# Kernel optimization log

Hardware: AMD Instinct MI355X
Metric: run time of the kernel (lower is better)

Reference implementation:

```python
import jax, jax.numpy as jnp
import numpy as np

B, L, d, D = 256, 128, 2, 128  # batch, sites, local dim, bond dim


def setup_inputs() -> dict:
    key = jax.random.key(0)
    k1, k2 = jax.random.split(key)
    # local quantum-number indices (output of hilbert.states_to_local_indices)
    x = jax.random.randint(k1, (B, L), 0, d, dtype=jnp.int32)
    # MPS unit-cell tensors: kernel_init (normal, std=0.01) + identity, as in setup()
    tensors = 0.01 * jax.random.normal(k2, (L, d, D, D), dtype=jnp.float32) \
        + jnp.eye(D, dtype=jnp.float32)
    return {"x": x, "tensors": tensors}


def reference(x, tensors):
    # x: (B, L) int indices in [0, d); tensors: (L, d, D, D)
    # symperiod == L so the tile in __call__ is a no-op.
    Bn, Ln = x.shape
    Dn = tensors.shape[-1]
    edge0 = jnp.broadcast_to(jnp.eye(Dn, dtype=tensors.dtype), (Bn, Dn, Dn))

    @jax.checkpoint
    def step(edge, pair):
        site_tensors, qn = pair          # (d, D, D), (B,)
        a = site_tensors[qn]             # gather per-sample matrix -> (B, D, D)
        return edge @ a, None            # batched (B,D,D)@(B,D,D)

    edge, _ = jax.lax.scan(step, edge0, (tensors, x.T))
    psi = jnp.trace(edge, axis1=-2, axis2=-1)     # (B,)
    return jnp.log(psi.astype(jnp.complex64))
```

## Files before the change

### kernel.cpp

```cpp
#include <hip/hip_runtime.h>
#include <cstdint>

#define DD   128
#define LL   128
#define MAT  (DD*DD)
#define ROWB 256

typedef float  f32x16 __attribute__((ext_vector_type(16)));
typedef short  bf16x8 __attribute__((ext_vector_type(8)));
typedef unsigned short u16_t;

__device__ u16_t g_A  [LL*2*MAT];
__device__ u16_t g_At [LL*2*MAT];
__device__ u16_t g_M2 [64*4*MAT];
__device__ u16_t g_M2t[64*4*MAT];
__device__ u16_t g_M4t[32*16*MAT];
__device__ u16_t g_F0 [256*MAT];
__device__ u16_t g_F1 [256*MAT];

__device__ __forceinline__ u16_t f2bf(float f){
  unsigned int x = __builtin_bit_cast(unsigned int, f);
  unsigned int r = (x + 0x7FFFu + ((x >> 16) & 1u)) >> 16;
  return (u16_t)r;
}
__device__ __forceinline__ float bf2f(u16_t u){
  unsigned int x = ((unsigned int)u) << 16;
  return __builtin_bit_cast(float, x);
}
__device__ __forceinline__ f32x16 mfma32(bf16x8 a, bf16x8 b, f32x16 c){
  return __builtin_amdgcn_mfma_f32_32x32x16_bf16(a, b, c, 0, 0, 0);
}
__device__ __forceinline__ f32x16 zero16(){
  f32x16 z;
#pragma unroll
  for (int i = 0; i < 16; ++i) z[i] = 0.f;
  return z;
}
__device__ __forceinline__ unsigned cvtpk(float lo, float hi){
  unsigned r;
  asm("v_cvt_pk_bf16_f32 %0, %1, %2" : "=v"(r) : "v"(lo), "v"(hi));
  return r;
}
__device__ __forceinline__ void pl32swap(unsigned &a, unsigned &b){
  asm volatile("v_permlane32_swap_b32 %0, %1" : "+v"(a), "+v"(b));
}

__device__ __forceinline__ void stage32k(char* dstLds, const u16_t* srcG, int ltid){
  int w4 = ltid >> 6, l = ltid & 63;
  const char* g = (const char*)srcG + w4*8192 + l*16;
  char* s = dstLds + w4*8192;
#pragma unroll
  for (int i = 0; i < 8; ++i){
    __builtin_amdgcn_global_load_lds(
      (const __attribute__((address_space(1))) unsigned int*)(uintptr_t)(g + i*1024),
      (__attribute__((address_space(3))) unsigned int*)(unsigned int)(uintptr_t)(s + i*1024),
      16, 0, 0);
  }
}

__global__ __launch_bounds__(256, 1) void k_convert(const float* __restrict__ T){
  __shared__ float tile[128][129];
  const int lq = blockIdx.x, tid = threadIdx.x;
  const float* src = T + (size_t)lq * MAT;
#pragma unroll 4
  for (int i = 0; i < 64; ++i){
    int idx = tid + 256*i;
    float v = src[idx];
    g_A[lq*MAT + idx] = f2bf(v);
    tile[idx >> 7][idx & 127] = v;
  }
  __syncthreads();
#pragma unroll 4
  for (int i = 0; i < 64; ++i){
    int idx = tid + 256*i;
    int c = idx >> 7, k = idx & 127;
    g_At[lq*MAT + idx] = f2bf(tile[k][c]);
  }
}

__global__ __launch_bounds__(256, 1) void k_prod(int level){
  __shared__ u16_t CT[MAT];
  __shared__ u16_t CR[MAT];
  const int bid = blockIdx.x, tid = threadIdx.x;
  const int w = tid >> 6, lane = tid & 63, g = lane >> 5, ln = lane & 31;
  const int wr = (w >> 1) * 64, wc = (w & 1) * 64;

  const u16_t *X, *Yt; u16_t *Z, *Zt;
  if (level == 1){
    int p = bid >> 2, c2 = bid & 3;
    X  = g_A  + ((2*p)*2   + (c2 & 1)) * MAT;
    Yt = g_At + ((2*p+1)*2 + ((c2 >> 1) & 1)) * MAT;
    Z  = g_M2  + bid*MAT;
    Zt = g_M2t + bid*MAT;
  } else {
    int gg = bid >> 4, c = bid & 15;
    X  = g_M2  + ((2*gg)*4   + (c & 3)) * MAT;
    Yt = g_M2t + ((2*gg+1)*4 + (c >> 2)) * MAT;
    Z  = nullptr;
    Zt = g_M4t + bid*MAT;
  }

  f32x16 acc[2][2];
  acc[0][0] = zero16(); acc[0][1] = zero16();
  acc[1][0] = zero16(); acc[1][1] = zero16();

#pragma unroll
  for (int kw = 0; kw < 8; ++kw){
    int ko = kw*32 + g*16;
    bf16x8 a0 = *(const bf16x8*)((const char*)X  + (wr + ln     )*ROWB + ko);
    bf16x8 a1 = *(const bf16x8*)((const char*)X  + (wr + 32 + ln)*ROWB + ko);
    bf16x8 b0 = *(const bf16x8*)((const char*)Yt + (wc + ln     )*ROWB + ko);
    bf16x8 b1 = *(const bf16x8*)((const char*)Yt + (wc + 32 + ln)*ROWB + ko);
    acc[0][0] = mfma32(a0, b0, acc[0][0]);
    acc[0][1] = mfma32(a0, b1, acc[0][1]);
    acc[1][0] = mfma32(a1, b0, acc[1][0]);
    acc[1][1] = mfma32(a1, b1, acc[1][1]);
  }

#pragma unroll
  for (int mt = 0; mt < 2; ++mt){
#pragma unroll
    for (int nt = 0; nt < 2; ++nt){
      int c  = wc + nt*32 + ln;
      int xc = (c & 15) << 4;
#pragma unroll
      for (int q = 0; q < 4; ++q){
        int r4 = wr + mt*32 + 8*q + 4*g;
        unsigned int lo = (unsigned)f2bf(acc[mt][nt][4*q+0]) | ((unsigned)f2bf(acc[mt][nt][4*q+1]) << 16);
        unsigned int hi = (unsigned)f2bf(acc[mt][nt][4*q+2]) | ((unsigned)f2bf(acc[mt][nt][4*q+3]) << 16);
        uint2 v; v.x = lo; v.y = hi;
        *(uint2*)((char*)CT + c*ROWB + ((2*r4) ^ xc)) = v;
      }
      if (level == 1){
#pragma unroll
        for (int i = 0; i < 16; ++i){
          int r = wr + mt*32 + (i & 3) + 8*(i >> 2) + 4*g;
          *(u16_t*)((char*)CR + r*ROWB + ((2*c) ^ ((r & 15) << 4))) = f2bf(acc[mt][nt][i]);
        }
      }
    }
  }
  __syncthreads();

  if (level == 1){
#pragma unroll
    for (int i = 0; i < 8; ++i){
      int o = (tid + 256*i) * 16;
      int row = o >> 8, wb = o & 255;
      int xr = (row & 15) << 4;
      uint4 vt = *(const uint4*)((const char*)CT + row*ROWB + (wb ^ xr));
      *(uint4*)((char*)Zt + o) = vt;
      uint4 vz = *(const uint4*)((const char*)CR + row*ROWB + (wb ^ xr));
      *(uint4*)((char*)Z + o) = vz;
    }
  } else {
#pragma unroll
    for (int i = 0; i < 8; ++i){
      int o = tid + 256*i;
      int lnn = o & 31, ggg = (o >> 5) & 1, kww = (o >> 6) & 7, rtt = o >> 9;
      int r = 32*rtt + lnn;
      int srcB = r*ROWB + ((32*kww + 16*ggg) ^ ((r & 15) << 4));
      uint4 vt = *(const uint4*)((const char*)CT + srcB);
      *(uint4*)((char*)Zt + o*16) = vt;
    }
  }
}

#define LDS_MAIN (2*32768 + 64)

__global__ __launch_bounds__(256, 1) void k_main(const int* __restrict__ x){
  extern __shared__ char lds[];
  char* bufs  = lds;
  int*  combo = (int*)(lds + 2*32768);

  const int bid = blockIdx.x;
  const int b = bid & 255, half = bid >> 8;
  const int tid = threadIdx.x;
  const int w = tid >> 6, lane = tid & 63, g = lane >> 5, ln = lane & 31;

  if (tid < 16){
    const int* xb = x + b*LL + (half*16 + tid)*4;
    combo[tid] = (xb[0] & 1) | ((xb[1] & 1) << 1) | ((xb[2] & 1) << 2) | ((xb[3] & 1) << 3);
  }

  uint4 F[8];
#pragma unroll
  for (int kw = 0; kw < 8; ++kw){
    unsigned wd[4] = {0u,0u,0u,0u};
#pragma unroll
    for (int j = 0; j < 8; ++j){
      int k = 16*kw + 8*g + j;
      if (k == 32*w + ln) wd[j >> 1] |= 0x3F80u << (16*(j & 1));
    }
    uint4 v; v.x = wd[0]; v.y = wd[1]; v.z = wd[2]; v.w = wd[3];
    F[kw] = v;
  }
  __syncthreads();

  stage32k(bufs, g_M4t + (size_t)((half*16)*16 + combo[0])*MAT, tid);
  __syncthreads();

  for (int s = 0; s < 16; ++s){
    const char* Mc = bufs + (s & 1)*32768;
    char*       Mn = bufs + ((s + 1) & 1)*32768;
    if (s + 1 < 16){
      stage32k(Mn, g_M4t + (size_t)((half*16 + s + 1)*16 + combo[s+1])*MAT, tid);
    }

    const char* Ml = Mc + lane*16;

    f32x16 acc[4];
#pragma unroll
    for (int rt = 0; rt < 4; ++rt) acc[rt] = zero16();

#pragma unroll
    for (int kw = 0; kw < 8; ++kw){
      bf16x8 bb = __builtin_bit_cast(bf16x8, F[kw]);
#pragma unroll
      for (int rt = 0; rt < 4; ++rt){
        bf16x8 a = *(const bf16x8*)(Ml + (rt*8 + kw)*1024);
        acc[rt] = mfma32(a, bb, acc[rt]);
      }
    }

#pragma unroll
    for (int rt = 0; rt < 4; ++rt){
      unsigned y0 = cvtpk(acc[rt][0],  acc[rt][1]);
      unsigned x0 = cvtpk(acc[rt][4],  acc[rt][5]);
      pl32swap(y0, x0);
      unsigned y1 = cvtpk(acc[rt][2],  acc[rt][3]);
      unsigned x1 = cvtpk(acc[rt][6],  acc[rt][7]);
      pl32swap(y1, x1);
      uint4 v0; v0.x = y0; v0.y = y1; v0.z = x0; v0.w = x1;
      F[2*rt] = v0;

      unsigned y2 = cvtpk(acc[rt][8],  acc[rt][9]);
      unsigned x2 = cvtpk(acc[rt][12], acc[rt][13]);
      pl32swap(y2, x2);
      unsigned y3 = cvtpk(acc[rt][10], acc[rt][11]);
      unsigned x3 = cvtpk(acc[rt][14], acc[rt][15]);
      pl32swap(y3, x3);
      uint4 v1; v1.x = y2; v1.y = y3; v1.z = x2; v1.w = x3;
      F[2*rt+1] = v1;
    }
    __syncthreads();
  }

  const int c = 32*w + ln;
  if (half == 0){
    u16_t* dst = g_F0 + (size_t)b*MAT + c*128;
#pragma unroll
    for (int kw = 0; kw < 8; ++kw)
      *(uint4*)(dst + kw*16 + g*8) = F[kw];
  } else {
    u16_t* dst = g_F1 + (size_t)b*MAT + c;
#pragma unroll
    for (int kw = 0; kw < 8; ++kw){
      uint4 v = F[kw];
      unsigned wd[4] = {v.x, v.y, v.z, v.w};
#pragma unroll
      for (int j = 0; j < 8; ++j){
        int k = 16*kw + 8*g + j;
        u16_t bits = (u16_t)((j & 1) ? (wd[j >> 1] >> 16) : (wd[j >> 1] & 0xFFFF));
        dst[(size_t)k*128] = bits;
      }
    }
  }
}

__global__ __launch_bounds__(256, 1) void k_tail(float* __restrict__ out,
                                                 int out_complex){
  __shared__ float red[4];
  const int b = blockIdx.x, tid = threadIdx.x;
  const int w = tid >> 6, lane = tid & 63;

  const u16_t* S0 = g_F0 + (size_t)b*MAT;
  const u16_t* W  = g_F1 + (size_t)b*MAT;

  float sum = 0.f;
#pragma unroll
  for (int i = 0; i < 8; ++i){
    int o = (i*256 + tid)*8;
    uint4 a = *(const uint4*)(S0 + o);
    uint4 v = *(const uint4*)(W  + o);
    unsigned aw[4] = {a.x, a.y, a.z, a.w};
    unsigned vw[4] = {v.x, v.y, v.z, v.w};
#pragma unroll
    for (int q = 0; q < 4; ++q){
      sum += bf2f((u16_t)(aw[q] & 0xFFFF)) * bf2f((u16_t)(vw[q] & 0xFFFF));
      sum += bf2f((u16_t)(aw[q] >> 16))    * bf2f((u16_t)(vw[q] >> 16));
    }
  }
#pragma unroll
  for (int off = 1; off < 64; off <<= 1) sum += __shfl_xor(sum, off, 64);
  if (lane == 0) red[w] = sum;
  __syncthreads();
  if (tid == 0){
    float s = red[0] + red[1] + red[2] + red[3];
    float re = logf(fabsf(s));
    float im = (s < 0.f) ? 3.14159265358979323f : 0.f;
    if (out_complex){ out[2*b] = re; out[2*b+1] = im; }
    else            { out[b] = re; }
  }
}

extern "C" void kernel_launch(void* const* d_in, const int* in_sizes, int n_in,
                              void* d_out, int out_size, void* d_ws, size_t ws_size,
                              hipStream_t stream){
  const int*   x = (const int*)d_in[0];
  const float* T = (const float*)d_in[1];
  int Bn = in_sizes[0] / LL;
  int oc = (out_size >= 2*Bn) ? 1 : 0;

  (void)d_ws; (void)ws_size; (void)n_in;
  hipFuncSetAttribute(reinterpret_cast<const void*>(k_main),
                      hipFuncAttributeMaxDynamicSharedMemorySize, LDS_MAIN);

  k_convert<<<LL*2,  256, 0, stream>>>(T);
  k_prod   <<<256,   256, 0, stream>>>(1);
  k_prod   <<<512,   256, 0, stream>>>(2);
  k_main   <<<2*Bn,  256, LDS_MAIN, stream>>>(x);
  k_tail   <<<Bn,    256, 0, stream>>>((float*)d_out, oc);
}
```

Measured before the change: 76.93 us.

## Split chain product into four quarters per sample and combine with MFMA tail

Each sample's 128-site chain product is now split across four blocks of 32 sites instead of two blocks of 64. Each block streams half-matrix 16KB chunks in a double-buffered loop, with smaller LDS and launch bounds allowing four blocks per CU. The tail kernel now does two 128x128 bf16 matrix products per sample with MFMA and computes the trace of their product via elementwise dot. This raises parallelism and occupancy in the main kernel. In exchange it adds a heavier tail kernel, more global scratch traffic, and an extra bf16 rounding stage.

```diff
diff --git a/kernel.cpp b/kernel.cpp
--- a/kernel.cpp
+++ b/kernel.cpp
@@ -17,6 +17,8 @@
 __device__ u16_t g_M4t[32*16*MAT];
 __device__ u16_t g_F0 [256*MAT];
 __device__ u16_t g_F1 [256*MAT];
+__device__ u16_t g_F2 [256*MAT];
+__device__ u16_t g_F3 [256*MAT];
 
 __device__ __forceinline__ u16_t f2bf(float f){
   unsigned int x = __builtin_bit_cast(unsigned int, f);
@@ -45,12 +47,12 @@
   asm volatile("v_permlane32_swap_b32 %0, %1" : "+v"(a), "+v"(b));
 }
 
-__device__ __forceinline__ void stage32k(char* dstLds, const u16_t* srcG, int ltid){
-  int w4 = ltid >> 6, l = ltid & 63;
-  const char* g = (const char*)srcG + w4*8192 + l*16;
-  char* s = dstLds + w4*8192;
-#pragma unroll
-  for (int i = 0; i < 8; ++i){
+__device__ __forceinline__ void stage16k(char* dstLds, const u16_t* srcG, int tid){
+  int w4 = tid >> 6, l = tid & 63;
+  const char* g = (const char*)srcG + w4*4096 + l*16;
+  char* s = dstLds + w4*4096;
+#pragma unroll
+  for (int i = 0; i < 4; ++i){
     __builtin_amdgcn_global_load_lds(
       (const __attribute__((address_space(1))) unsigned int*)(uintptr_t)(g + i*1024),
       (__attribute__((address_space(3))) unsigned int*)(unsigned int)(uintptr_t)(s + i*1024),
@@ -166,22 +168,18 @@
   }
 }
 
-#define LDS_MAIN (2*32768 + 64)
-
-__global__ __launch_bounds__(256, 1) void k_main(const int* __restrict__ x){
+#define LDS_MAIN (2*16384)
+
+__global__ __launch_bounds__(256, 4) void k_main(const int* __restrict__ x){
   extern __shared__ char lds[];
-  char* bufs  = lds;
-  int*  combo = (int*)(lds + 2*32768);
 
   const int bid = blockIdx.x;
-  const int b = bid & 255, half = bid >> 8;
+  const int b = bid & 255, q = bid >> 8;
   const int tid = threadIdx.x;
   const int w = tid >> 6, lane = tid & 63, g = lane >> 5, ln = lane & 31;
 
-  if (tid < 16){
-    const int* xb = x + b*LL + (half*16 + tid)*4;
-    combo[tid] = (xb[0] & 1) | ((xb[1] & 1) << 1) | ((xb[2] & 1) << 2) | ((xb[3] & 1) << 3);
-  }
+  int xv = x[b*LL + q*32 + (lane & 31)] & 1;
+  unsigned long long bits = __ballot(xv != 0);
 
   uint4 F[8];
 #pragma unroll
@@ -195,65 +193,72 @@
     uint4 v; v.x = wd[0]; v.y = wd[1]; v.z = wd[2]; v.w = wd[3];
     F[kw] = v;
   }
+
+  {
+    int cb0 = (int)(bits & 15ull);
+    stage16k(lds, g_M4t + (size_t)((q*8)*16 + cb0)*MAT, tid);
+  }
   __syncthreads();
 
-  stage32k(bufs, g_M4t + (size_t)((half*16)*16 + combo[0])*MAT, tid);
-  __syncthreads();
-
-  for (int s = 0; s < 16; ++s){
-    const char* Mc = bufs + (s & 1)*32768;
-    char*       Mn = bufs + ((s + 1) & 1)*32768;
-    if (s + 1 < 16){
-      stage32k(Mn, g_M4t + (size_t)((half*16 + s + 1)*16 + combo[s+1])*MAT, tid);
-    }
-
-    const char* Ml = Mc + lane*16;
-
-    f32x16 acc[4];
-#pragma unroll
-    for (int rt = 0; rt < 4; ++rt) acc[rt] = zero16();
+  f32x16 acc[4];
+  for (int p = 0; p < 16; ++p){
+    if ((p & 1) == 0){
+#pragma unroll
+      for (int rt = 0; rt < 4; ++rt) acc[rt] = zero16();
+    }
+    if (p + 1 < 16){
+      int it = (p + 1) >> 1, h = (p + 1) & 1;
+      int cb = (int)((bits >> (4*it)) & 15ull);
+      stage16k(lds + ((p + 1) & 1)*16384,
+               g_M4t + (size_t)((q*8 + it)*16 + cb)*MAT + h*8192, tid);
+    }
+
+    const char* Ml = lds + (p & 1)*16384 + lane*16;
+    const int h = p & 1;
 
 #pragma unroll
     for (int kw = 0; kw < 8; ++kw){
       bf16x8 bb = __builtin_bit_cast(bf16x8, F[kw]);
 #pragma unroll
+      for (int d = 0; d < 2; ++d){
+        bf16x8 a = *(const bf16x8*)(Ml + (d*8 + kw)*1024);
+        acc[2*h + d] = mfma32(a, bb, acc[2*h + d]);
+      }
+    }
+
+    if (p & 1){
+#pragma unroll
       for (int rt = 0; rt < 4; ++rt){
-        bf16x8 a = *(const bf16x8*)(Ml + (rt*8 + kw)*1024);
-        acc[rt] = mfma32(a, bb, acc[rt]);
-      }
-    }
-
-#pragma unroll
-    for (int rt = 0; rt < 4; ++rt){
-      unsigned y0 = cvtpk(acc[rt][0],  acc[rt][1]);
-      unsigned x0 = cvtpk(acc[rt][4],  acc[rt][5]);
-      pl32swap(y0, x0);
-      unsigned y1 = cvtpk(acc[rt][2],  acc[rt][3]);
-      unsigned x1 = cvtpk(acc[rt][6],  acc[rt][7]);
-      pl32swap(y1, x1);
-      uint4 v0; v0.x = y0; v0.y = y1; v0.z = x0; v0.w = x1;
-      F[2*rt] = v0;
-
-      unsigned y2 = cvtpk(acc[rt][8],  acc[rt][9]);
-      unsigned x2 = cvtpk(acc[rt][12], acc[rt][13]);
-      pl32swap(y2, x2);
-      unsigned y3 = cvtpk(acc[rt][10], acc[rt][11]);
-      unsigned x3 = cvtpk(acc[rt][14], acc[rt][15]);
-      pl32swap(y3, x3);
-      uint4 v1; v1.x = y2; v1.y = y3; v1.z = x2; v1.w = x3;
-      F[2*rt+1] = v1;
+        unsigned y0 = cvtpk(acc[rt][0],  acc[rt][1]);
+        unsigned x0 = cvtpk(acc[rt][4],  acc[rt][5]);
+        pl32swap(y0, x0);
+        unsigned y1 = cvtpk(acc[rt][2],  acc[rt][3]);
+        unsigned x1 = cvtpk(acc[rt][6],  acc[rt][7]);
+        pl32swap(y1, x1);
+        uint4 v0; v0.x = y0; v0.y = y1; v0.z = x0; v0.w = x1;
+        F[2*rt] = v0;
+
+        unsigned y2 = cvtpk(acc[rt][8],  acc[rt][9]);
+        unsigned x2 = cvtpk(acc[rt][12], acc[rt][13]);
+        pl32swap(y2, x2);
+        unsigned y3 = cvtpk(acc[rt][10], acc[rt][11]);
+        unsigned x3 = cvtpk(acc[rt][14], acc[rt][15]);
+        pl32swap(y3, x3);
+        uint4 v1; v1.x = y2; v1.y = y3; v1.z = x2; v1.w = x3;
+        F[2*rt+1] = v1;
+      }
     }
     __syncthreads();
   }
 
   const int c = 32*w + ln;
-  if (half == 0){
-    u16_t* dst = g_F0 + (size_t)b*MAT + c*128;
+  if ((q & 1) == 0){
+    u16_t* dst = (q == 0 ? g_F0 : g_F2) + (size_t)b*MAT + c*128;
 #pragma unroll
     for (int kw = 0; kw < 8; ++kw)
       *(uint4*)(dst + kw*16 + g*8) = F[kw];
   } else {
-    u16_t* dst = g_F1 + (size_t)b*MAT + c;
+    u16_t* dst = (q == 1 ? g_F1 : g_F3) + (size_t)b*MAT + c;
 #pragma unroll
     for (int kw = 0; kw < 8; ++kw){
       uint4 v = F[kw];
@@ -261,36 +266,62 @@
 #pragma unroll
       for (int j = 0; j < 8; ++j){
         int k = 16*kw + 8*g + j;
-        u16_t bits = (u16_t)((j & 1) ? (wd[j >> 1] >> 16) : (wd[j >> 1] & 0xFFFF));
-        dst[(size_t)k*128] = bits;
-      }
-    }
-  }
-}
-
-__global__ __launch_bounds__(256, 1) void k_tail(float* __restrict__ out,
-                                                 int out_complex){
+        u16_t bb = (u16_t)((j & 1) ? (wd[j >> 1] >> 16) : (wd[j >> 1] & 0xFFFF));
+        dst[(size_t)k*128] = bb;
+      }
+    }
+  }
+}
+
+__global__ __launch_bounds__(256, 1) void k_tail2(float* __restrict__ out,
+                                                  int out_complex){
   __shared__ float red[4];
   const int b = blockIdx.x, tid = threadIdx.x;
-  const int w = tid >> 6, lane = tid & 63;
-
-  const u16_t* S0 = g_F0 + (size_t)b*MAT;
-  const u16_t* W  = g_F1 + (size_t)b*MAT;
+  const int w = tid >> 6, lane = tid & 63, g = lane >> 5, ln = lane & 31;
+  const int wr = (w >> 1) * 64, wc = (w & 1) * 64;
+
+  const u16_t* X1  = g_F0 + (size_t)b*MAT;
+  const u16_t* Y1t = g_F1 + (size_t)b*MAT;
+  const u16_t* X2  = g_F3 + (size_t)b*MAT;
+  const u16_t* Y2t = g_F2 + (size_t)b*MAT;
+
+  f32x16 ap[2][2], ar[2][2];
+#pragma unroll
+  for (int mt = 0; mt < 2; ++mt)
+#pragma unroll
+    for (int nt = 0; nt < 2; ++nt){ ap[mt][nt] = zero16(); ar[mt][nt] = zero16(); }
+
+#pragma unroll
+  for (int kw = 0; kw < 8; ++kw){
+    int ko = kw*32 + g*16;
+    bf16x8 a0 = *(const bf16x8*)((const char*)X1  + (wr + ln     )*ROWB + ko);
+    bf16x8 a1 = *(const bf16x8*)((const char*)X1  + (wr + 32 + ln)*ROWB + ko);
+    bf16x8 b0 = *(const bf16x8*)((const char*)Y1t + (wc + ln     )*ROWB + ko);
+    bf16x8 b1 = *(const bf16x8*)((const char*)Y1t + (wc + 32 + ln)*ROWB + ko);
+    ap[0][0] = mfma32(a0, b0, ap[0][0]);
+    ap[0][1] = mfma32(a0, b1, ap[0][1]);
+    ap[1][0] = mfma32(a1, b0, ap[1][0]);
+    ap[1][1] = mfma32(a1, b1, ap[1][1]);
+
+    bf16x8 c0 = *(const bf16x8*)((const char*)X2  + (wr + ln     )*ROWB + ko);
+    bf16x8 c1 = *(const bf16x8*)((const char*)X2  + (wr + 32 + ln)*ROWB + ko);
+    bf16x8 d0 = *(const bf16x8*)((const char*)Y2t + (wc + ln     )*ROWB + ko);
+    bf16x8 d1 = *(const bf16x8*)((const char*)Y2t + (wc + 32 + ln)*ROWB + ko);
+    ar[0][0] = mfma32(c0, d0, ar[0][0]);
+    ar[0][1] = mfma32(c0, d1, ar[0][1]);
+    ar[1][0] = mfma32(c1, d0, ar[1][0]);
+    ar[1][1] = mfma32(c1, d1, ar[1][1]);
+  }
 
   float sum = 0.f;
 #pragma unroll
-  for (int i = 0; i < 8; ++i){
-    int o = (i*256 + tid)*8;
-    uint4 a = *(const uint4*)(S0 + o);
-    uint4 v = *(const uint4*)(W  + o);
-    unsigned aw[4] = {a.x, a.y, a.z, a.w};
-    unsigned vw[4] = {v.x, v.y, v.z, v.w};
-#pragma unroll
-    for (int q = 0; q < 4; ++q){
-      sum += bf2f((u16_t)(aw[q] & 0xFFFF)) * bf2f((u16_t)(vw[q] & 0xFFFF));
-      sum += bf2f((u16_t)(aw[q] >> 16))    * bf2f((u16_t)(vw[q] >> 16));
-    }
-  }
+  for (int mt = 0; mt < 2; ++mt)
+#pragma unroll
+    for (int nt = 0; nt < 2; ++nt)
+#pragma unroll
+      for (int i = 0; i < 16; ++i)
+        sum += ap[mt][nt][i] * ar[mt][nt][i];
+
 #pragma unroll
   for (int off = 1; off < 64; off <<= 1) sum += __shfl_xor(sum, off, 64);
   if (lane == 0) red[w] = sum;
@@ -319,6 +350,6 @@
   k_convert<<<LL*2,  256, 0, stream>>>(T);
   k_prod   <<<256,   256, 0, stream>>>(1);
   k_prod   <<<512,   256, 0, stream>>>(2);
-  k_main   <<<2*Bn,  256, LDS_MAIN, stream>>>(x);
-  k_tail   <<<Bn,    256, 0, stream>>>((float*)d_out, oc);
-}
+  k_main   <<<4*Bn,  256, LDS_MAIN, stream>>>(x);
+  k_tail2  <<<Bn,    256, 0, stream>>>((float*)d_out, oc);
+}
```

After: 304.8 us. 296% more time.
